# Kernel optimization log

Hardware: AMD Instinct MI355X
Metric: run time of the kernel (lower is better)

## Reference

```python
import jax, jax.numpy as jnp
import numpy as np

NUM_CHUNKS = 8
TOP_K = 2
IN_FEATURES = 4096
OUT_FEATURES = 4096
CIN = IN_FEATURES // NUM_CHUNKS    # 512
COUT = OUT_FEATURES // NUM_CHUNKS  # 512
BATCH = 8192


def setup_inputs() -> dict:
    key = jax.random.key(0)
    kx, kw, kb = jax.random.split(key, 3)
    x = jax.random.normal(kx, (BATCH, IN_FEATURES), dtype=jnp.float32)
    # per-chunk Linear params: W[i] is [out_chunk, in_chunk] like nn.Linear.weight
    bound = 1.0 / np.sqrt(CIN)
    W = jax.random.uniform(kw, (NUM_CHUNKS, COUT, CIN), jnp.float32, -bound, bound)
    b = jax.random.uniform(kb, (NUM_CHUNKS, COUT), jnp.float32, -bound, bound)
    return {"x": x, "W": W, "b": b}


def reference(x, W, b):
    B = x.shape[0]
    nc, cout, cin = W.shape
    # split into equal chunks along feature dim: [B, nc, cin]
    xr = x.reshape(B, nc, cin)
    # per-chunk activity: mean |x| over batch and chunk features -> [nc]
    activities = jnp.mean(jnp.abs(xr), axis=(0, 2))
    # select top-k most active chunks (indices are constants w.r.t. grads)
    _, idx = jax.lax.top_k(activities, TOP_K)  # [k]
    xs = xr[:, idx, :]                          # [B, k, cin]
    # grouped GEMM only on selected chunks: y = x @ W^T + b
    ys = jnp.einsum('bki,koi->bko', xs, W[idx]) + b[idx][None]  # [B, k, cout]
    out = jnp.zeros((B, nc, cout), dtype=x.dtype).at[:, idx, :].set(ys)
    return out.reshape(B, nc * cout), activities
```

## Files before the change

### kernel.cpp

```cpp
#include <hip/hip_runtime.h>
#include <hip/hip_bf16.h>

#define BATCH 8192
#define NCH 8
#define CIN 512
#define COUT 512
#define NF 4096

typedef __attribute__((ext_vector_type(8))) __bf16 bf16x8;
typedef __attribute__((ext_vector_type(4))) float f32x4;

__global__ __launch_bounds__(256) void act_kernel(const float* __restrict__ x,
                                                  float* __restrict__ sums) {
    const int c = blockIdx.y;
    const int rbase = blockIdx.x * 32;
    const int t = threadIdx.x;
    const int rhalf = t >> 7;
    const int colq = (t & 127) << 2;
    const float* base = x + (size_t)rbase * NF + c * CIN;
    float s = 0.f;
#pragma unroll
    for (int p = 0; p < 16; ++p) {
        const int r = p * 2 + rhalf;
        const float4 v = *(const float4*)(base + (size_t)r * NF + colq);
        s += fabsf(v.x) + fabsf(v.y) + fabsf(v.z) + fabsf(v.w);
    }
#pragma unroll
    for (int off = 32; off > 0; off >>= 1) s += __shfl_down(s, off, 64);
    __shared__ float red[4];
    const int lane = t & 63, wv = t >> 6;
    if (lane == 0) red[wv] = s;
    __syncthreads();
    if (t == 0) atomicAdd(&sums[c], red[0] + red[1] + red[2] + red[3]);
}

__global__ void topk_kernel(const float* __restrict__ sums,
                            float* __restrict__ out_act,
                            int* __restrict__ idx_out) {
    if (threadIdx.x == 0) {
        const float scale = 1.0f / ((float)BATCH * (float)CIN);
        float a[NCH];
        for (int i = 0; i < NCH; ++i) { a[i] = sums[i] * scale; out_act[i] = a[i]; }
        int i0 = 0;
        for (int i = 1; i < NCH; ++i) if (a[i] > a[i0]) i0 = i;
        int i1 = (i0 == 0) ? 1 : 0;
        for (int i = 0; i < NCH; ++i) if (i != i0 && a[i] > a[i1]) i1 = i;
        idx_out[0] = i0; idx_out[1] = i1;
    }
}

__global__ __launch_bounds__(256) void gemm_kernel(const float* __restrict__ x,
                                                   const float* __restrict__ W,
                                                   const float* __restrict__ bias,
                                                   const int* __restrict__ idx,
                                                   float* __restrict__ out) {
    const int c = blockIdx.z;
    const int i0 = idx[0], i1 = idx[1];
    const int t = threadIdx.x;
    const size_t obase = (size_t)(blockIdx.x * 128) * NF + c * COUT + blockIdx.y * 128;

    if (c != i0 && c != i1) {
        const float4 z = make_float4(0.f, 0.f, 0.f, 0.f);
        const int rq = t >> 5;
        const int cq = (t & 31) << 2;
#pragma unroll
        for (int p = 0; p < 16; ++p)
            *(float4*)(out + obase + (size_t)(p * 8 + rq) * NF + cq) = z;
        return;
    }

    __shared__ __bf16 Xs[128][40];
    __shared__ __bf16 Ws[128][40];

    const int lane = t & 63, w = t >> 6;
    const int wm = (w >> 1) * 64, wn = (w & 1) * 64;
    const int lr = lane & 15, lq = lane >> 4;

    f32x4 acc[4][4];
#pragma unroll
    for (int i = 0; i < 4; ++i)
#pragma unroll
        for (int j = 0; j < 4; ++j) acc[i][j] = (f32x4){0.f, 0.f, 0.f, 0.f};

    const int srow = t >> 1;
    const int scol = (t & 1) * 16;
    const float* xg = x + (size_t)(blockIdx.x * 128 + srow) * NF + c * CIN + scol;
    const float* wg = W + ((size_t)c * COUT + blockIdx.y * 128 + srow) * CIN + scol;

    for (int kk = 0; kk < CIN; kk += 32) {
        {
            const float4 a0 = *(const float4*)(xg + kk + 0);
            const float4 a1 = *(const float4*)(xg + kk + 4);
            const float4 a2 = *(const float4*)(xg + kk + 8);
            const float4 a3 = *(const float4*)(xg + kk + 12);
            bf16x8 p0, p1;
            p0[0] = (__bf16)a0.x; p0[1] = (__bf16)a0.y; p0[2] = (__bf16)a0.z; p0[3] = (__bf16)a0.w;
            p0[4] = (__bf16)a1.x; p0[5] = (__bf16)a1.y; p0[6] = (__bf16)a1.z; p0[7] = (__bf16)a1.w;
            p1[0] = (__bf16)a2.x; p1[1] = (__bf16)a2.y; p1[2] = (__bf16)a2.z; p1[3] = (__bf16)a2.w;
            p1[4] = (__bf16)a3.x; p1[5] = (__bf16)a3.y; p1[6] = (__bf16)a3.z; p1[7] = (__bf16)a3.w;
            *(bf16x8*)&Xs[srow][scol]     = p0;
            *(bf16x8*)&Xs[srow][scol + 8] = p1;
        }
        {
            const float4 a0 = *(const float4*)(wg + kk + 0);
            const float4 a1 = *(const float4*)(wg + kk + 4);
            const float4 a2 = *(const float4*)(wg + kk + 8);
            const float4 a3 = *(const float4*)(wg + kk + 12);
            bf16x8 p0, p1;
            p0[0] = (__bf16)a0.x; p0[1] = (__bf16)a0.y; p0[2] = (__bf16)a0.z; p0[3] = (__bf16)a0.w;
            p0[4] = (__bf16)a1.x; p0[5] = (__bf16)a1.y; p0[6] = (__bf16)a1.z; p0[7] = (__bf16)a1.w;
            p1[0] = (__bf16)a2.x; p1[1] = (__bf16)a2.y; p1[2] = (__bf16)a2.z; p1[3] = (__bf16)a2.w;
            p1[4] = (__bf16)a3.x; p1[5] = (__bf16)a3.y; p1[6] = (__bf16)a3.z; p1[7] = (__bf16)a3.w;
            *(bf16x8*)&Ws[srow][scol]     = p0;
            *(bf16x8*)&Ws[srow][scol + 8] = p1;
        }
        __syncthreads();

        bf16x8 av[4], bv[4];
#pragma unroll
        for (int mt = 0; mt < 4; ++mt) av[mt] = *(const bf16x8*)&Xs[wm + mt * 16 + lr][lq * 8];
#pragma unroll
        for (int nt = 0; nt < 4; ++nt) bv[nt] = *(const bf16x8*)&Ws[wn + nt * 16 + lr][lq * 8];
#pragma unroll
        for (int mt = 0; mt < 4; ++mt)
#pragma unroll
            for (int nt = 0; nt < 4; ++nt)
                acc[mt][nt] = __builtin_amdgcn_mfma_f32_16x16x32_bf16(av[mt], bv[nt], acc[mt][nt], 0, 0, 0);
        __syncthreads();
    }

    float bvv[4];
#pragma unroll
    for (int nt = 0; nt < 4; ++nt)
        bvv[nt] = bias[c * COUT + blockIdx.y * 128 + wn + nt * 16 + lr];
#pragma unroll
    for (int mt = 0; mt < 4; ++mt)
#pragma unroll
        for (int nt = 0; nt < 4; ++nt)
#pragma unroll
            for (int r = 0; r < 4; ++r) {
                const int row = wm + mt * 16 + lq * 4 + r;
                const int col = wn + nt * 16 + lr;
                out[obase + (size_t)row * NF + col] = acc[mt][nt][r] + bvv[nt];
            }
}

extern "C" void kernel_launch(void* const* d_in, const int* in_sizes, int n_in,
                              void* d_out, int out_size, void* d_ws, size_t ws_size,
                              hipStream_t stream) {
    const float* x = (const float*)d_in[0];
    const float* W = (const float*)d_in[1];
    const float* b = (const float*)d_in[2];
    float* out = (float*)d_out;
    float* sums = (float*)d_ws;
    int* idx = (int*)((char*)d_ws + NCH * sizeof(float));

    hipMemsetAsync(d_ws, 0, NCH * sizeof(float), stream);
    act_kernel<<<dim3(256, NCH), 256, 0, stream>>>(x, sums);
    topk_kernel<<<1, 64, 0, stream>>>(sums, out + (size_t)BATCH * NF, idx);
    gemm_kernel<<<dim3(64, 4, NCH), 256, 0, stream>>>(x, W, b, idx, out);
}
```

Before: 276.6 us.

## Pre-convert x and W to bf16 in the activity pass and stream tiles via LDS DMA

The activity-reduction kernel now also writes a bf16 copy of every x chunk, and extra blocks convert W to bf16, all into workspace. The GEMM then loads bf16 tiles straight into LDS with global_load_lds instead of loading fp32 and converting in registers. This removes per-tile conversion work and halves GEMM input bytes. In exchange it writes bf16 copies of all eight chunks although only two are used, adding substantial write traffic, and the unpadded LDS layout may cause bank conflicts.

Result: no change. 275.6 us (-0.4%).

```diff
diff --git a/kernel.cpp b/kernel.cpp
--- a/kernel.cpp
+++ b/kernel.cpp
@@ -10,20 +10,55 @@
 typedef __attribute__((ext_vector_type(8))) __bf16 bf16x8;
 typedef __attribute__((ext_vector_type(4))) float f32x4;
 
-__global__ __launch_bounds__(256) void act_kernel(const float* __restrict__ x,
-                                                  float* __restrict__ sums) {
+__device__ __forceinline__ void async_load16(const void* g, void* l) {
+    __builtin_amdgcn_global_load_lds((const __attribute__((address_space(1))) void*)g,
+                                     (__attribute__((address_space(3))) void*)l, 16, 0, 0);
+}
+
+__device__ __forceinline__ bf16x8 cvt8(const float4 a, const float4 b) {
+    bf16x8 p;
+    p[0] = (__bf16)a.x; p[1] = (__bf16)a.y; p[2] = (__bf16)a.z; p[3] = (__bf16)a.w;
+    p[4] = (__bf16)b.x; p[5] = (__bf16)b.y; p[6] = (__bf16)b.z; p[7] = (__bf16)b.w;
+    return p;
+}
+
+__global__ __launch_bounds__(256) void prep_kernel(const float* __restrict__ x,
+                                                   const float* __restrict__ W,
+                                                   __bf16* __restrict__ xbf,
+                                                   __bf16* __restrict__ wbf,
+                                                   float* __restrict__ sums) {
     const int c = blockIdx.y;
-    const int rbase = blockIdx.x * 32;
+    const int bx = blockIdx.x;
     const int t = threadIdx.x;
-    const int rhalf = t >> 7;
-    const int colq = (t & 127) << 2;
-    const float* base = x + (size_t)rbase * NF + c * CIN;
+
+    if (bx >= 256) {
+        const int q = bx - 256;
+        const float* src = W + (size_t)c * (COUT * CIN) + q * 32768;
+        __bf16* dst = wbf + (size_t)c * (COUT * CIN) + q * 32768;
+#pragma unroll
+        for (int p = 0; p < 16; ++p) {
+            const int off = p * 2048 + t * 8;
+            const float4 a0 = *(const float4*)(src + off);
+            const float4 a1 = *(const float4*)(src + off + 4);
+            *(bf16x8*)(dst + off) = cvt8(a0, a1);
+        }
+        return;
+    }
+
+    const int rsub = t >> 6;
+    const int col = (t & 63) * 8;
+    const size_t rbase = (size_t)bx * 32;
+    __bf16* xc = xbf + (size_t)c * BATCH * CIN;
     float s = 0.f;
 #pragma unroll
-    for (int p = 0; p < 16; ++p) {
-        const int r = p * 2 + rhalf;
-        const float4 v = *(const float4*)(base + (size_t)r * NF + colq);
-        s += fabsf(v.x) + fabsf(v.y) + fabsf(v.z) + fabsf(v.w);
+    for (int p = 0; p < 8; ++p) {
+        const size_t r = rbase + p * 4 + rsub;
+        const float* src = x + r * NF + c * CIN + col;
+        const float4 a0 = *(const float4*)(src);
+        const float4 a1 = *(const float4*)(src + 4);
+        s += fabsf(a0.x) + fabsf(a0.y) + fabsf(a0.z) + fabsf(a0.w)
+           + fabsf(a1.x) + fabsf(a1.y) + fabsf(a1.z) + fabsf(a1.w);
+        *(bf16x8*)(xc + r * CIN + col) = cvt8(a0, a1);
     }
 #pragma unroll
     for (int off = 32; off > 0; off >>= 1) s += __shfl_down(s, off, 64);
@@ -49,17 +84,16 @@
     }
 }
 
-__global__ __launch_bounds__(256) void gemm_kernel(const float* __restrict__ x,
-                                                   const float* __restrict__ W,
+__global__ __launch_bounds__(256) void gemm_kernel(const __bf16* __restrict__ xbf,
+                                                   const __bf16* __restrict__ wbf,
                                                    const float* __restrict__ bias,
                                                    const int* __restrict__ idx,
                                                    float* __restrict__ out) {
     const int c = blockIdx.z;
-    const int i0 = idx[0], i1 = idx[1];
     const int t = threadIdx.x;
     const size_t obase = (size_t)(blockIdx.x * 128) * NF + c * COUT + blockIdx.y * 128;
 
-    if (c != i0 && c != i1) {
+    if (c != idx[0] && c != idx[1]) {
         const float4 z = make_float4(0.f, 0.f, 0.f, 0.f);
         const int rq = t >> 5;
         const int cq = (t & 31) << 2;
@@ -69,12 +103,21 @@
         return;
     }
 
-    __shared__ __bf16 Xs[128][40];
-    __shared__ __bf16 Ws[128][40];
+    __shared__ __bf16 Xs[128 * 32];
+    __shared__ __bf16 Wsh[128 * 32];
 
     const int lane = t & 63, w = t >> 6;
     const int wm = (w >> 1) * 64, wn = (w & 1) * 64;
     const int lr = lane & 15, lq = lane >> 4;
+
+    const int srow = lane >> 2;
+    const int skcol = (lane & 3) * 8;
+    const __bf16* xg = xbf + (size_t)c * BATCH * CIN
+                     + (size_t)(blockIdx.x * 128 + w * 32 + srow) * CIN + skcol;
+    const __bf16* wg = wbf + (size_t)c * COUT * CIN
+                     + (size_t)(blockIdx.y * 128 + w * 32 + srow) * CIN + skcol;
+    __bf16* xls = &Xs[(w * 32) * 32];
+    __bf16* wls = &Wsh[(w * 32) * 32];
 
     f32x4 acc[4][4];
 #pragma unroll
@@ -82,45 +125,18 @@
 #pragma unroll
         for (int j = 0; j < 4; ++j) acc[i][j] = (f32x4){0.f, 0.f, 0.f, 0.f};
 
-    const int srow = t >> 1;
-    const int scol = (t & 1) * 16;
-    const float* xg = x + (size_t)(blockIdx.x * 128 + srow) * NF + c * CIN + scol;
-    const float* wg = W + ((size_t)c * COUT + blockIdx.y * 128 + srow) * CIN + scol;
-
     for (int kk = 0; kk < CIN; kk += 32) {
-        {
-            const float4 a0 = *(const float4*)(xg + kk + 0);
-            const float4 a1 = *(const float4*)(xg + kk + 4);
-            const float4 a2 = *(const float4*)(xg + kk + 8);
-            const float4 a3 = *(const float4*)(xg + kk + 12);
-            bf16x8 p0, p1;
-            p0[0] = (__bf16)a0.x; p0[1] = (__bf16)a0.y; p0[2] = (__bf16)a0.z; p0[3] = (__bf16)a0.w;
-            p0[4] = (__bf16)a1.x; p0[5] = (__bf16)a1.y; p0[6] = (__bf16)a1.z; p0[7] = (__bf16)a1.w;
-            p1[0] = (__bf16)a2.x; p1[1] = (__bf16)a2.y; p1[2] = (__bf16)a2.z; p1[3] = (__bf16)a2.w;
-            p1[4] = (__bf16)a3.x; p1[5] = (__bf16)a3.y; p1[6] = (__bf16)a3.z; p1[7] = (__bf16)a3.w;
-            *(bf16x8*)&Xs[srow][scol]     = p0;
-            *(bf16x8*)&Xs[srow][scol + 8] = p1;
-        }
-        {
-            const float4 a0 = *(const float4*)(wg + kk + 0);
-            const float4 a1 = *(const float4*)(wg + kk + 4);
-            const float4 a2 = *(const float4*)(wg + kk + 8);
-            const float4 a3 = *(const float4*)(wg + kk + 12);
-            bf16x8 p0, p1;
-            p0[0] = (__bf16)a0.x; p0[1] = (__bf16)a0.y; p0[2] = (__bf16)a0.z; p0[3] = (__bf16)a0.w;
-            p0[4] = (__bf16)a1.x; p0[5] = (__bf16)a1.y; p0[6] = (__bf16)a1.z; p0[7] = (__bf16)a1.w;
-            p1[0] = (__bf16)a2.x; p1[1] = (__bf16)a2.y; p1[2] = (__bf16)a2.z; p1[3] = (__bf16)a2.w;
-            p1[4] = (__bf16)a3.x; p1[5] = (__bf16)a3.y; p1[6] = (__bf16)a3.z; p1[7] = (__bf16)a3.w;
-            *(bf16x8*)&Ws[srow][scol]     = p0;
-            *(bf16x8*)&Ws[srow][scol + 8] = p1;
-        }
+        async_load16(xg + kk, xls);
+        async_load16(xg + kk + (size_t)16 * CIN, xls + 16 * 32);
+        async_load16(wg + kk, wls);
+        async_load16(wg + kk + (size_t)16 * CIN, wls + 16 * 32);
         __syncthreads();
 
         bf16x8 av[4], bv[4];
 #pragma unroll
-        for (int mt = 0; mt < 4; ++mt) av[mt] = *(const bf16x8*)&Xs[wm + mt * 16 + lr][lq * 8];
+        for (int mt = 0; mt < 4; ++mt) av[mt] = *(const bf16x8*)&Xs[(wm + mt * 16 + lr) * 32 + lq * 8];
 #pragma unroll
-        for (int nt = 0; nt < 4; ++nt) bv[nt] = *(const bf16x8*)&Ws[wn + nt * 16 + lr][lq * 8];
+        for (int nt = 0; nt < 4; ++nt) bv[nt] = *(const bf16x8*)&Wsh[(wn + nt * 16 + lr) * 32 + lq * 8];
 #pragma unroll
         for (int mt = 0; mt < 4; ++mt)
 #pragma unroll
@@ -152,11 +168,14 @@
     const float* W = (const float*)d_in[1];
     const float* b = (const float*)d_in[2];
     float* out = (float*)d_out;
+
     float* sums = (float*)d_ws;
-    int* idx = (int*)((char*)d_ws + NCH * sizeof(float));
+    int* idx = (int*)((char*)d_ws + 32);
+    __bf16* xbf = (__bf16*)((char*)d_ws + 256);
+    __bf16* wbf = (__bf16*)((char*)d_ws + 256 + (size_t)BATCH * NF * 2);
 
-    hipMemsetAsync(d_ws, 0, NCH * sizeof(float), stream);
-    act_kernel<<<dim3(256, NCH), 256, 0, stream>>>(x, sums);
+    hipMemsetAsync(d_ws, 0, 64, stream);
+    prep_kernel<<<dim3(264, NCH), 256, 0, stream>>>(x, W, xbf, wbf, sums);
     topk_kernel<<<1, 64, 0, stream>>>(sums, out + (size_t)BATCH * NF, idx);
-    gemm_kernel<<<dim3(64, 4, NCH), 256, 0, stream>>>(x, W, b, idx, out);
+    gemm_kernel<<<dim3(64, 4, NCH), 256, 0, stream>>>(xbf, wbf, b, idx, out);
 }
```
